# Optimization experiments

Hardware: AMD Instinct MI355X
Metric: run time of the kernel (lower is better)

## Reference

```python
import jax, jax.numpy as jnp
import numpy as np

D = 1024
B = 16384

def setup_inputs() -> dict:
    key = jax.random.key(0)
    ks = jax.random.split(key, 8)
    s = 1.0 / np.sqrt(D)  # torch Linear default init scale (uniform), use scaled normal
    return {
        "f1": jax.random.normal(ks[0], (B, D), jnp.float32),
        "f2": jax.random.normal(ks[1], (B, D), jnp.float32),
        "Wq": jax.random.normal(ks[2], (D, D), jnp.float32) * s,
        "bq": jax.random.normal(ks[3], (D,), jnp.float32) * s,
        "Wk": jax.random.normal(ks[4], (D, D), jnp.float32) * s,
        "bk": jax.random.normal(ks[5], (D,), jnp.float32) * s,
        "Wv": jax.random.normal(ks[6], (D, D), jnp.float32) * s,
        "bv": jax.random.normal(ks[7], (D,), jnp.float32) * s,
    }

def reference(f1, f2, Wq, bq, Wk, bk, Wv, bv):
    d = f1.shape[-1]
    feats = jnp.stack([f1, f2], axis=1)          # [B, 2, D]
    # nn.Linear: y = x @ W.T + b
    Q = jnp.einsum("bsd,ed->bse", feats, Wq) + bq  # [B, 2, D]
    K = jnp.einsum("bsd,ed->bse", feats, Wk) + bk
    V = jnp.einsum("bsd,ed->bse", feats, Wv) + bv
    scores = jnp.einsum("bse,bte->bst", Q, K) / jnp.sqrt(jnp.asarray(d, feats.dtype))  # [B, 2, 2]
    attn = jax.nn.softmax(scores, axis=-1)
    attended = jnp.einsum("bst,btd->bsd", attn, V)  # [B, 2, D]
    return attended.sum(axis=1)                     # [B, D]
```

## Files before the change

kernel.cpp:

```cpp
#include <hip/hip_runtime.h>
#include <hip/hip_bf16.h>
#include <stdint.h>

typedef unsigned short u16;
typedef __bf16 bf16x8 __attribute__((ext_vector_type(8)));
typedef float f32x4 __attribute__((ext_vector_type(4)));

#define D_DIM 1024
#define B_ROWS 16384
#define M_ROWS 32768
#define BM 128
#define BN 128
#define BK 64

__device__ __forceinline__ u16 f2bs(float f) {
    union { float f; unsigned u; } v; v.f = f;
    unsigned r = v.u + 0x7FFFu + ((v.u >> 16) & 1u);
    return (u16)(r >> 16);
}
__device__ __forceinline__ float bs2f(unsigned bits16) {
    union { unsigned u; float f; } v; v.u = bits16 << 16;
    return v.f;
}
__device__ __forceinline__ float bidx(uint2 v, int e) {
    unsigned w = (e < 2) ? v.x : v.y;
    unsigned sh = (unsigned)(e & 1) * 16u;
    return bs2f((w >> sh) & 0xFFFFu);
}
__device__ __forceinline__ uint2 pack4(float4 f) {
    uint2 r;
    r.x = (unsigned)f2bs(f.x) | ((unsigned)f2bs(f.y) << 16);
    r.y = (unsigned)f2bs(f.z) | ((unsigned)f2bs(f.w) << 16);
    return r;
}

#define GLD16(gsrc, ldst)                                                      \
    __builtin_amdgcn_global_load_lds(                                          \
        (const __attribute__((address_space(1))) void*)(gsrc),                 \
        (__attribute__((address_space(3))) void*)(ldst), 16, 0, 0)

#define MFMA16(a, b, c) __builtin_amdgcn_mfma_f32_16x16x32_bf16((a), (b), (c), 0, 0, 0)

__global__ __launch_bounds__(256) void cvt_feats(const float* __restrict__ f1,
                                                 const float* __restrict__ f2,
                                                 u16* __restrict__ X) {
    size_t i4   = (size_t)blockIdx.x * 256 + threadIdx.x;
    size_t base = i4 * 4;
    size_t brow = base >> 10;
    size_t col  = base & 1023;
    float4 a = *(const float4*)(f1 + base);
    float4 b = *(const float4*)(f2 + base);
    *(uint2*)(X + (2 * brow) * D_DIM + col)     = pack4(a);
    *(uint2*)(X + (2 * brow + 1) * D_DIM + col) = pack4(b);
}

__global__ __launch_bounds__(256) void cvt_wv(const float* __restrict__ Wv,
                                              u16* __restrict__ Wvb) {
    size_t base = ((size_t)blockIdx.x * 256 + threadIdx.x) * 4;
    *(uint2*)(Wvb + base) = pack4(*(const float4*)(Wv + base));
}

__global__ __launch_bounds__(256) void transpose_bf16(const float* __restrict__ in,
                                                      u16* __restrict__ out) {
    __shared__ float lds[32][33];
    const int tx = threadIdx.x & 31;
    const int ty = threadIdx.x >> 5;
    const int r0 = (blockIdx.x >> 5) * 32;
    const int c0 = (blockIdx.x & 31) * 32;
#pragma unroll
    for (int i = 0; i < 4; ++i) {
        int r = ty + i * 8;
        lds[r][tx] = in[(size_t)(r0 + r) * D_DIM + c0 + tx];
    }
    __syncthreads();
#pragma unroll
    for (int i = 0; i < 4; ++i) {
        int r = ty + i * 8;
        out[(size_t)(c0 + r) * D_DIM + r0 + tx] = f2bs(lds[tx][r]);
    }
}

__global__ __launch_bounds__(256) void uvc_k(const float* __restrict__ Wq,
                                             const float* __restrict__ Wk,
                                             const float* __restrict__ bq,
                                             const float* __restrict__ bk,
                                             float* __restrict__ u,
                                             float* __restrict__ v,
                                             float* __restrict__ cbuf) {
    const int dl = threadIdx.x & 31;
    const int fg = threadIdx.x >> 5;
    const int d  = blockIdx.x * 32 + dl;
    float au = 0.f, av = 0.f;
    const int f0 = fg * 128;
    for (int f = f0; f < f0 + 128; ++f) {
        au = fmaf(Wq[(size_t)f * D_DIM + d], bk[f], au);
        av = fmaf(Wk[(size_t)f * D_DIM + d], bq[f], av);
    }
    __shared__ float su[8][32], sv[8][32];
    su[fg][dl] = au; sv[fg][dl] = av;
    __syncthreads();
    if (fg == 0) {
        float a = 0.f, b2 = 0.f;
#pragma unroll
        for (int g = 0; g < 8; ++g) { a += su[g][dl]; b2 += sv[g][dl]; }
        u[d] = a; v[d] = b2;
    }
    if (blockIdx.x == 0) {
        __shared__ float red[256];
        float p = 0.f;
        for (int f = threadIdx.x; f < D_DIM; f += 256) p = fmaf(bq[f], bk[f], p);
        red[threadIdx.x] = p;
        __syncthreads();
        for (int s = 128; s; s >>= 1) {
            if (threadIdx.x < s) red[threadIdx.x] += red[threadIdx.x + s];
            __syncthreads();
        }
        if (threadIdx.x == 0) cbuf[0] = red[0];
    }
}

__global__ __launch_bounds__(256, 3) void gemm_small(const u16* __restrict__ A,
                                                     const u16* __restrict__ W,
                                                     u16* __restrict__ C, int ncols) {
    constexpr int K = D_DIM;
    __shared__ u16 As[BM * BK];
    __shared__ u16 Bs[BN * BK];

    const int cpx  = gridDim.x >> 3;
    const int orig = (blockIdx.x & 7) * cpx + (blockIdx.x >> 3);
    const int nTn = ncols / BN;
    const int m0 = (orig / nTn) * BM, n0 = (orig % nTn) * BN;

    const int tid  = threadIdx.x;
    const int lane = tid & 63;
    const int wave = tid >> 6;
    const int wr = wave >> 1, wc = wave & 1;
    const int lr = lane & 15;
    const int kg = lane >> 4;

    f32x4 acc[4][4] = {};

    const int sr  = tid >> 3;
    const int scs = ((tid & 7) ^ ((tid >> 3) & 7)) * 8;
    const u16* aRow = A + (size_t)(m0 + sr) * K + scs;
    const u16* bRow = W + (size_t)(n0 + sr) * K + scs;
    u16* aDst = As + tid * 8;
    u16* bDst = Bs + tid * 8;

    for (int kt = 0; kt < K; kt += BK) {
#pragma unroll
        for (int i = 0; i < 4; ++i) {
            GLD16(aRow + (size_t)i * 32 * K + kt, aDst + i * 2048);
            GLD16(bRow + (size_t)i * 32 * K + kt, bDst + i * 2048);
        }
        __syncthreads();
#pragma unroll
        for (int kk = 0; kk < 2; ++kk) {
            bf16x8 af[4], bfr[4];
            const int kx = kk * 4 + kg;
#pragma unroll
            for (int mf = 0; mf < 4; ++mf) {
                const int R = wr * 64 + mf * 16 + lr;
                af[mf] = *(const bf16x8*)(As + R * 64 + ((kx ^ (R & 7)) * 8));
            }
#pragma unroll
            for (int nf = 0; nf < 4; ++nf) {
                const int S = wc * 64 + nf * 16 + lr;
                bfr[nf] = *(const bf16x8*)(Bs + S * 64 + ((kx ^ (S & 7)) * 8));
            }
#pragma unroll
            for (int mf = 0; mf < 4; ++mf)
#pragma unroll
                for (int nf = 0; nf < 4; ++nf)
                    acc[mf][nf] = MFMA16(af[mf], bfr[nf], acc[mf][nf]);
        }
        __syncthreads();
    }

    const int cr = (lane >> 4) * 4;
    const int cc = lane & 15;
#pragma unroll
    for (int mf = 0; mf < 4; ++mf)
#pragma unroll
        for (int nf = 0; nf < 4; ++nf) {
            int col = n0 + wc * 64 + nf * 16 + cc;
#pragma unroll
            for (int j = 0; j < 4; ++j) {
                int row = m0 + wr * 64 + mf * 16 + cr + j;
                C[(size_t)row * ncols + col] = f2bs(acc[mf][nf][j]);
            }
        }
}

template<bool FUSED>
__global__ __launch_bounds__(512, 2) void gemm8p(const u16* __restrict__ A,
                                                 const u16* __restrict__ W,
                                                 const float* __restrict__ bias,
                                                 u16* __restrict__ C,
                                                 const float2* __restrict__ wts,
                                                 float* __restrict__ out,
                                                 int ncols) {
    constexpr int K  = D_DIM;
    constexpr int NT = K / 64;
    __shared__ u16 L[65536];

    const int cpx  = gridDim.x >> 3;
    const int orig = (blockIdx.x & 7) * cpx + (blockIdx.x >> 3);
    const int nTn  = ncols >> 8;
    const int m0 = (orig / nTn) << 8, n0 = (orig % nTn) << 8;

    const int tid  = threadIdx.x;
    const int lane = tid & 63;
    const int wid  = tid >> 6;
    const int wm = wid >> 2, wn = wid & 3;
    const int lr = lane & 15;
    const int kg = lane >> 4;
    const int r7 = lr & 7;
    const int cx0 = ((0 + kg) ^ r7) * 8;
    const int cx1 = ((4 + kg) ^ r7) * 8;
    const int sS  = (wn & 1) * 64;

    const int rb  = tid >> 3;
    const int scs = ((tid & 7) ^ (rb & 7)) * 8;
    const u16* aB = A + (size_t)(m0 + rb) * K + scs;
    const u16* bB = W + (size_t)(n0 + rb) * K + scs;
    u16* aD = L + tid * 8;
    u16* bD = L + 32768 + tid * 8;

#define ST_HALF(tile, h)                                                       \
    {                                                                          \
        const int d_ = (tile) & 1;                                             \
        const size_t ko_ = (size_t)(tile) * 64;                                \
        if ((h) < 2) {                                                         \
            const u16* s_ = aB + (size_t)(h) * 128 * K + ko_;                  \
            u16* t_ = aD + (d_ * 2 + (h)) * 8192;                              \
            GLD16(s_, t_);                                                     \
            GLD16(s_ + (size_t)64 * K, t_ + 4096);                            \
        } else {                                                               \
            const u16* s_ = bB + (size_t)((h) - 2) * 128 * K + ko_;            \
            u16* t_ = bD + (d_ * 2 + ((h) - 2)) * 8192;                        \
            GLD16(s_, t_);                                                     \
            GLD16(s_ + (size_t)64 * K, t_ + 4096);                            \
        }                                                                      \
    }

    f32x4 acc[8][4] = {};
    bf16x8 af[8][2], bf[4][2];

#pragma unroll
    for (int h = 0; h < 4; ++h) ST_HALF(0, h);
#pragma unroll
    for (int h = 0; h < 4; ++h) ST_HALF(1, h);
    asm volatile("s_waitcnt vmcnt(8)" ::: "memory");
    __builtin_amdgcn_s_barrier();

#pragma unroll 2
    for (int t = 0; t < NT; ++t) {
        const int d = t & 1;
        const u16* Ab = L + (d * 2 + wm) * 8192;
        const u16* Bb = L + 32768 + (d * 2 + (wn >> 1)) * 8192;
        const bool more = (t + 2 < NT);

#pragma unroll
        for (int m = 0; m < 4; ++m) {
            const int R = m * 16 + lr;
            af[m][0] = *(const bf16x8*)(Ab + R * 64 + cx0);
            af[m][1] = *(const bf16x8*)(Ab + R * 64 + cx1);
        }
#pragma unroll
        for (int n = 0; n < 2; ++n) {
            const int S = sS + n * 16 + lr;
            bf[n][0] = *(const bf16x8*)(Bb + S * 64 + cx0);
            bf[n][1] = *(const bf16x8*)(Bb + S * 64 + cx1);
        }
        __builtin_amdgcn_s_barrier();
        __builtin_amdgcn_s_setprio(1);
#pragma unroll
        for (int m = 0; m < 4; ++m)
#pragma unroll
            for (int n = 0; n < 2; ++n) {
                acc[m][n] = MFMA16(af[m][0], bf[n][0], acc[m][n]);
                acc[m][n] = MFMA16(af[m][1], bf[n][1], acc[m][n]);
            }
        __builtin_amdgcn_s_setprio(0);
        __builtin_amdgcn_s_barrier();

#pragma unroll
        for (int n = 2; n < 4; ++n) {
            const int S = sS + n * 16 + lr;
            bf[n][0] = *(const bf16x8*)(Bb + S * 64 + cx0);
            bf[n][1] = *(const bf16x8*)(Bb + S * 64 + cx1);
        }
        __builtin_amdgcn_s_barrier();
        __builtin_amdgcn_s_setprio(1);
#pragma unroll
        for (int m = 0; m < 4; ++m)
#pragma unroll
            for (int n = 2; n < 4; ++n) {
                acc[m][n] = MFMA16(af[m][0], bf[n][0], acc[m][n]);
                acc[m][n] = MFMA16(af[m][1], bf[n][1], acc[m][n]);
            }
        __builtin_amdgcn_s_setprio(0);
        __builtin_amdgcn_s_barrier();

#pragma unroll
        for (int m = 4; m < 8; ++m) {
            const int R = m * 16 + lr;
            af[m][0] = *(const bf16x8*)(Ab + R * 64 + cx0);
            af[m][1] = *(const bf16x8*)(Ab + R * 64 + cx1);
        }
        if (more) { ST_HALF(t + 2, 2); ST_HALF(t + 2, 3); }
        __builtin_amdgcn_s_barrier();
        __builtin_amdgcn_s_setprio(1);
#pragma unroll
        for (int m = 4; m < 8; ++m)
#pragma unroll
            for (int n = 0; n < 2; ++n) {
                acc[m][n] = MFMA16(af[m][0], bf[n][0], acc[m][n]);
                acc[m][n] = MFMA16(af[m][1], bf[n][1], acc[m][n]);
            }
        __builtin_amdgcn_s_setprio(0);
        __builtin_amdgcn_s_barrier();

        if (more) { ST_HALF(t + 2, 0); ST_HALF(t + 2, 1); }
        __builtin_amdgcn_s_barrier();
        __builtin_amdgcn_s_setprio(1);
#pragma unroll
        for (int m = 4; m < 8; ++m)
#pragma unroll
            for (int n = 2; n < 4; ++n) {
                acc[m][n] = MFMA16(af[m][0], bf[n][0], acc[m][n]);
                acc[m][n] = MFMA16(af[m][1], bf[n][1], acc[m][n]);
            }
        __builtin_amdgcn_s_setprio(0);
        if (more) asm volatile("s_waitcnt vmcnt(8)" ::: "memory");
        else      asm volatile("s_waitcnt vmcnt(0)" ::: "memory");
        __builtin_amdgcn_s_barrier();
    }
#undef ST_HALF

    const int cr = (lane >> 4) * 4;
    const int cc = lane & 15;
    if constexpr (!FUSED) {
#pragma unroll
        for (int mf = 0; mf < 8; ++mf)
#pragma unroll
            for (int nf = 0; nf < 4; ++nf) {
                int col = n0 + wn * 64 + nf * 16 + cc;
                float bsv = bias ? bias[col] : 0.f;
#pragma unroll
                for (int j = 0; j < 4; ++j) {
                    int row = m0 + wm * 128 + mf * 16 + cr + j;
                    C[(size_t)row * ncols + col] = f2bs(acc[mf][nf][j] + bsv);
                }
            }
    } else {
#pragma unroll
        for (int mf = 0; mf < 8; ++mf) {
            const int rowbase = m0 + wm * 128 + mf * 16 + cr;
            const int p0 = rowbase >> 1;
            const float2 w0 = wts[p0];
            const float2 w1 = wts[p0 + 1];
#pragma unroll
            for (int nf = 0; nf < 4; ++nf) {
                int col = n0 + wn * 64 + nf * 16 + cc;
                float bsv = bias[col];
                float o0 = w0.x * (acc[mf][nf][0] + bsv) + w0.y * (acc[mf][nf][1] + bsv);
                float o1 = w1.x * (acc[mf][nf][2] + bsv) + w1.y * (acc[mf][nf][3] + bsv);
                out[(size_t)p0 * D_DIM + col]       = o0;
                out[(size_t)(p0 + 1) * D_DIM + col] = o1;
            }
        }
    }
}

__global__ __launch_bounds__(256) void scores2(const u16* __restrict__ X,
                                               const u16* __restrict__ G,
                                               const float* __restrict__ u,
                                               const float* __restrict__ v,
                                               const float* __restrict__ cbuf,
                                               float2* __restrict__ wts) {
    const int wave = threadIdx.x >> 6;
    const int lane = threadIdx.x & 63;
    const size_t b = (size_t)blockIdx.x * 4 + wave;
    const u16* x0p = X + (2 * b) * D_DIM;
    const u16* x1p = x0p + D_DIM;
    const u16* g0p = G + (2 * b) * D_DIM;
    const u16* g1p = g0p + D_DIM;

    float d00 = 0.f, d01 = 0.f, d10 = 0.f, d11 = 0.f;
    float au0 = 0.f, au1 = 0.f, bv0 = 0.f, bv1 = 0.f;
#pragma unroll
    for (int s = 0; s < 4; ++s) {
        int c = s * 256 + lane * 4;
        uint2 x0 = *(const uint2*)(x0p + c);
        uint2 x1 = *(const uint2*)(x1p + c);
        uint2 g0 = *(const uint2*)(g0p + c);
        uint2 g1 = *(const uint2*)(g1p + c);
        float4 uu = *(const float4*)(u + c);
        float4 vv = *(const float4*)(v + c);
        float uA[4] = {uu.x, uu.y, uu.z, uu.w};
        float vA[4] = {vv.x, vv.y, vv.z, vv.w};
#pragma unroll
        for (int e = 0; e < 4; ++e) {
            float a0 = bidx(x0, e), a1 = bidx(x1, e);
            float c0 = bidx(g0, e), c1 = bidx(g1, e);
            d00 = fmaf(a0, c0, d00); d01 = fmaf(a0, c1, d01);
            d10 = fmaf(a1, c0, d10); d11 = fmaf(a1, c1, d11);
            au0 = fmaf(uA[e], a0, au0); au1 = fmaf(uA[e], a1, au1);
            bv0 = fmaf(vA[e], a0, bv0); bv1 = fmaf(vA[e], a1, bv1);
        }
    }
#pragma unroll
    for (int off = 32; off; off >>= 1) {
        d00 += __shfl_xor(d00, off); d01 += __shfl_xor(d01, off);
        d10 += __shfl_xor(d10, off); d11 += __shfl_xor(d11, off);
        au0 += __shfl_xor(au0, off); au1 += __shfl_xor(au1, off);
        bv0 += __shfl_xor(bv0, off); bv1 += __shfl_xor(bv1, off);
    }
    if (lane == 0) {
        const float cc0 = cbuf[0];
        const float sc = 1.0f / 32.0f;
        float s00 = (d00 + au0 + bv0 + cc0) * sc;
        float s01 = (d01 + au0 + bv1 + cc0) * sc;
        float s10 = (d10 + au1 + bv0 + cc0) * sc;
        float s11 = (d11 + au1 + bv1 + cc0) * sc;
        float mA = fmaxf(s00, s01);
        float e00 = expf(s00 - mA), e01 = expf(s01 - mA);
        float rA = 1.0f / (e00 + e01);
        float mB = fmaxf(s10, s11);
        float e10 = expf(s10 - mB), e11 = expf(s11 - mB);
        float rB = 1.0f / (e10 + e11);
        float2 w;
        w.x = e00 * rA + e10 * rB;
        w.y = e01 * rA + e11 * rB;
        wts[b] = w;
    }
}

extern "C" void kernel_launch(void* const* d_in, const int* in_sizes, int n_in,
                              void* d_out, int out_size, void* d_ws, size_t ws_size,
                              hipStream_t stream) {
    const float* f1 = (const float*)d_in[0];
    const float* f2 = (const float*)d_in[1];
    const float* Wq = (const float*)d_in[2];
    const float* bq = (const float*)d_in[3];
    const float* Wk = (const float*)d_in[4];
    const float* bk = (const float*)d_in[5];
    const float* Wv = (const float*)d_in[6];
    const float* bv = (const float*)d_in[7];
    float* out = (float*)d_out;

    char*   w    = (char*)d_ws;
    u16*    X    = (u16*)w;
    u16*    G    = X + (size_t)M_ROWS * D_DIM;
    u16*    Wvb  = G + (size_t)M_ROWS * D_DIM;
    u16*    WqT  = Wvb + (size_t)D_DIM * D_DIM;
    u16*    WkT  = WqT + (size_t)D_DIM * D_DIM;
    u16*    Mb   = WkT + (size_t)D_DIM * D_DIM;
    float*  u    = (float*)(Mb + (size_t)D_DIM * D_DIM);
    float*  v    = u + D_DIM;
    float*  cbuf = v + D_DIM;
    float2* wts  = (float2*)(cbuf + 64);

    cvt_feats<<<(B_ROWS * D_DIM / 4) / 256, 256, 0, stream>>>(f1, f2, X);
    cvt_wv<<<(D_DIM * D_DIM / 4) / 256, 256, 0, stream>>>(Wv, Wvb);
    transpose_bf16<<<1024, 256, 0, stream>>>(Wq, WqT);
    transpose_bf16<<<1024, 256, 0, stream>>>(Wk, WkT);
    uvc_k<<<D_DIM / 32, 256, 0, stream>>>(Wq, Wk, bq, bk, u, v, cbuf);

    gemm_small<<<(D_DIM / BM) * (D_DIM / BN), 256, 0, stream>>>(WqT, WkT, Mb, D_DIM);
    gemm8p<false><<<(M_ROWS / 256) * (D_DIM / 256), 512, 0, stream>>>(
        X, Mb, nullptr, G, nullptr, nullptr, D_DIM);
    scores2<<<B_ROWS / 4, 256, 0, stream>>>(X, G, u, v, cbuf, wts);
    gemm8p<true><<<(M_ROWS / 256) * (D_DIM / 256), 512, 0, stream>>>(
        X, Wvb, bv, nullptr, wts, out, D_DIM);
}
```

Measured before the change: 227.3 us.

## Mix feature rows by attention weights before V projection to halve V GEMM

Because the output is linear in V, the scores kernel now forms Z = w0*x0 + w1*x1 per batch row in bf16. The V projection then runs on B rows instead of 2B rows, with the bias added as 2*bv. This roughly halves the second large GEMM's FLOPs and removes the weighted fused epilogue. It costs an extra B×D bf16 write and read of Z, plus an additional bf16 rounding of the mixed features.

```diff
diff --git a/kernel.cpp b/kernel.cpp
--- a/kernel.cpp
+++ b/kernel.cpp
@@ -22,10 +22,9 @@
     union { unsigned u; float f; } v; v.u = bits16 << 16;
     return v.f;
 }
-__device__ __forceinline__ float bidx(uint2 v, int e) {
-    unsigned w = (e < 2) ? v.x : v.y;
-    unsigned sh = (unsigned)(e & 1) * 16u;
-    return bs2f((w >> sh) & 0xFFFFu);
+__device__ __forceinline__ float b8x(uint4 q, int e) {
+    unsigned w[4] = {q.x, q.y, q.z, q.w};
+    return bs2f((w[e >> 1] >> ((unsigned)(e & 1) * 16u)) & 0xFFFFu);
 }
 __device__ __forceinline__ uint2 pack4(float4 f) {
     uint2 r;
@@ -192,12 +191,11 @@
         }
 }
 
-template<bool FUSED>
+template<bool F32OUT>
 __global__ __launch_bounds__(512, 2) void gemm8p(const u16* __restrict__ A,
                                                  const u16* __restrict__ W,
                                                  const float* __restrict__ bias,
                                                  u16* __restrict__ C,
-                                                 const float2* __restrict__ wts,
                                                  float* __restrict__ out,
                                                  int ncols) {
     constexpr int K  = D_DIM;
@@ -341,45 +339,40 @@
 
     const int cr = (lane >> 4) * 4;
     const int cc = lane & 15;
-    if constexpr (!FUSED) {
+    if constexpr (!F32OUT) {
 #pragma unroll
         for (int mf = 0; mf < 8; ++mf)
 #pragma unroll
             for (int nf = 0; nf < 4; ++nf) {
                 int col = n0 + wn * 64 + nf * 16 + cc;
-                float bsv = bias ? bias[col] : 0.f;
 #pragma unroll
                 for (int j = 0; j < 4; ++j) {
                     int row = m0 + wm * 128 + mf * 16 + cr + j;
-                    C[(size_t)row * ncols + col] = f2bs(acc[mf][nf][j] + bsv);
+                    C[(size_t)row * ncols + col] = f2bs(acc[mf][nf][j]);
                 }
             }
     } else {
 #pragma unroll
-        for (int mf = 0; mf < 8; ++mf) {
-            const int rowbase = m0 + wm * 128 + mf * 16 + cr;
-            const int p0 = rowbase >> 1;
-            const float2 w0 = wts[p0];
-            const float2 w1 = wts[p0 + 1];
+        for (int mf = 0; mf < 8; ++mf)
 #pragma unroll
             for (int nf = 0; nf < 4; ++nf) {
                 int col = n0 + wn * 64 + nf * 16 + cc;
-                float bsv = bias[col];
-                float o0 = w0.x * (acc[mf][nf][0] + bsv) + w0.y * (acc[mf][nf][1] + bsv);
-                float o1 = w1.x * (acc[mf][nf][2] + bsv) + w1.y * (acc[mf][nf][3] + bsv);
-                out[(size_t)p0 * D_DIM + col]       = o0;
-                out[(size_t)(p0 + 1) * D_DIM + col] = o1;
-            }
-        }
-    }
-}
-
-__global__ __launch_bounds__(256) void scores2(const u16* __restrict__ X,
-                                               const u16* __restrict__ G,
-                                               const float* __restrict__ u,
-                                               const float* __restrict__ v,
-                                               const float* __restrict__ cbuf,
-                                               float2* __restrict__ wts) {
+                float bsv = 2.0f * bias[col];
+#pragma unroll
+                for (int j = 0; j < 4; ++j) {
+                    int row = m0 + wm * 128 + mf * 16 + cr + j;
+                    out[(size_t)row * ncols + col] = acc[mf][nf][j] + bsv;
+                }
+            }
+    }
+}
+
+__global__ __launch_bounds__(256) void scores_z(const u16* __restrict__ X,
+                                                const u16* __restrict__ G,
+                                                const float* __restrict__ u,
+                                                const float* __restrict__ v,
+                                                const float* __restrict__ cbuf,
+                                                u16* __restrict__ Z) {
     const int wave = threadIdx.x >> 6;
     const int lane = threadIdx.x & 63;
     const size_t b = (size_t)blockIdx.x * 4 + wave;
@@ -390,21 +383,24 @@
 
     float d00 = 0.f, d01 = 0.f, d10 = 0.f, d11 = 0.f;
     float au0 = 0.f, au1 = 0.f, bv0 = 0.f, bv1 = 0.f;
-#pragma unroll
-    for (int s = 0; s < 4; ++s) {
-        int c = s * 256 + lane * 4;
-        uint2 x0 = *(const uint2*)(x0p + c);
-        uint2 x1 = *(const uint2*)(x1p + c);
-        uint2 g0 = *(const uint2*)(g0p + c);
-        uint2 g1 = *(const uint2*)(g1p + c);
-        float4 uu = *(const float4*)(u + c);
-        float4 vv = *(const float4*)(v + c);
-        float uA[4] = {uu.x, uu.y, uu.z, uu.w};
-        float vA[4] = {vv.x, vv.y, vv.z, vv.w};
-#pragma unroll
-        for (int e = 0; e < 4; ++e) {
-            float a0 = bidx(x0, e), a1 = bidx(x1, e);
-            float c0 = bidx(g0, e), c1 = bidx(g1, e);
+    uint4 x0c[2], x1c[2];
+#pragma unroll
+    for (int s = 0; s < 2; ++s) {
+        const int c = s * 512 + lane * 8;
+        x0c[s] = *(const uint4*)(x0p + c);
+        x1c[s] = *(const uint4*)(x1p + c);
+        uint4 g0 = *(const uint4*)(g0p + c);
+        uint4 g1 = *(const uint4*)(g1p + c);
+        float4 uuA = *(const float4*)(u + c);
+        float4 uuB = *(const float4*)(u + c + 4);
+        float4 vvA = *(const float4*)(v + c);
+        float4 vvB = *(const float4*)(v + c + 4);
+        float uA[8] = {uuA.x, uuA.y, uuA.z, uuA.w, uuB.x, uuB.y, uuB.z, uuB.w};
+        float vA[8] = {vvA.x, vvA.y, vvA.z, vvA.w, vvB.x, vvB.y, vvB.z, vvB.w};
+#pragma unroll
+        for (int e = 0; e < 8; ++e) {
+            float a0 = b8x(x0c[s], e), a1 = b8x(x1c[s], e);
+            float c0 = b8x(g0, e),     c1 = b8x(g1, e);
             d00 = fmaf(a0, c0, d00); d01 = fmaf(a0, c1, d01);
             d10 = fmaf(a1, c0, d10); d11 = fmaf(a1, c1, d11);
             au0 = fmaf(uA[e], a0, au0); au1 = fmaf(uA[e], a1, au1);
@@ -418,23 +414,36 @@
         au0 += __shfl_xor(au0, off); au1 += __shfl_xor(au1, off);
         bv0 += __shfl_xor(bv0, off); bv1 += __shfl_xor(bv1, off);
     }
-    if (lane == 0) {
-        const float cc0 = cbuf[0];
-        const float sc = 1.0f / 32.0f;
-        float s00 = (d00 + au0 + bv0 + cc0) * sc;
-        float s01 = (d01 + au0 + bv1 + cc0) * sc;
-        float s10 = (d10 + au1 + bv0 + cc0) * sc;
-        float s11 = (d11 + au1 + bv1 + cc0) * sc;
-        float mA = fmaxf(s00, s01);
-        float e00 = expf(s00 - mA), e01 = expf(s01 - mA);
-        float rA = 1.0f / (e00 + e01);
-        float mB = fmaxf(s10, s11);
-        float e10 = expf(s10 - mB), e11 = expf(s11 - mB);
-        float rB = 1.0f / (e10 + e11);
-        float2 w;
-        w.x = e00 * rA + e10 * rB;
-        w.y = e01 * rA + e11 * rB;
-        wts[b] = w;
+    const float cc0 = cbuf[0];
+    const float sc = 1.0f / 32.0f;
+    float s00 = (d00 + au0 + bv0 + cc0) * sc;
+    float s01 = (d01 + au0 + bv1 + cc0) * sc;
+    float s10 = (d10 + au1 + bv0 + cc0) * sc;
+    float s11 = (d11 + au1 + bv1 + cc0) * sc;
+    float mA = fmaxf(s00, s01);
+    float e00 = expf(s00 - mA), e01 = expf(s01 - mA);
+    float rA = 1.0f / (e00 + e01);
+    float mB = fmaxf(s10, s11);
+    float e10 = expf(s10 - mB), e11 = expf(s11 - mB);
+    float rB = 1.0f / (e10 + e11);
+    const float w0 = e00 * rA + e10 * rB;
+    const float w1 = e01 * rA + e11 * rB;
+
+#pragma unroll
+    for (int s = 0; s < 2; ++s) {
+        const int c = s * 512 + lane * 8;
+        float4 lo, hi;
+        lo.x = w0 * b8x(x0c[s], 0) + w1 * b8x(x1c[s], 0);
+        lo.y = w0 * b8x(x0c[s], 1) + w1 * b8x(x1c[s], 1);
+        lo.z = w0 * b8x(x0c[s], 2) + w1 * b8x(x1c[s], 2);
+        lo.w = w0 * b8x(x0c[s], 3) + w1 * b8x(x1c[s], 3);
+        hi.x = w0 * b8x(x0c[s], 4) + w1 * b8x(x1c[s], 4);
+        hi.y = w0 * b8x(x0c[s], 5) + w1 * b8x(x1c[s], 5);
+        hi.z = w0 * b8x(x0c[s], 6) + w1 * b8x(x1c[s], 6);
+        hi.w = w0 * b8x(x0c[s], 7) + w1 * b8x(x1c[s], 7);
+        uint2 pl = pack4(lo), ph = pack4(hi);
+        uint4 o; o.x = pl.x; o.y = pl.y; o.z = ph.x; o.w = ph.y;
+        *(uint4*)(Z + b * D_DIM + c) = o;
     }
 }
 
@@ -454,14 +463,14 @@
     char*   w    = (char*)d_ws;
     u16*    X    = (u16*)w;
     u16*    G    = X + (size_t)M_ROWS * D_DIM;
-    u16*    Wvb  = G + (size_t)M_ROWS * D_DIM;
+    u16*    Z    = G + (size_t)M_ROWS * D_DIM;
+    u16*    Wvb  = Z + (size_t)B_ROWS * D_DIM;
     u16*    WqT  = Wvb + (size_t)D_DIM * D_DIM;
     u16*    WkT  = WqT + (size_t)D_DIM * D_DIM;
     u16*    Mb   = WkT + (size_t)D_DIM * D_DIM;
     float*  u    = (float*)(Mb + (size_t)D_DIM * D_DIM);
     float*  v    = u + D_DIM;
     float*  cbuf = v + D_DIM;
-    float2* wts  = (float2*)(cbuf + 64);
 
     cvt_feats<<<(B_ROWS * D_DIM / 4) / 256, 256, 0, stream>>>(f1, f2, X);
     cvt_wv<<<(D_DIM * D_DIM / 4) / 256, 256, 0, stream>>>(Wv, Wvb);
@@ -471,8 +480,8 @@
 
     gemm_small<<<(D_DIM / BM) * (D_DIM / BN), 256, 0, stream>>>(WqT, WkT, Mb, D_DIM);
     gemm8p<false><<<(M_ROWS / 256) * (D_DIM / 256), 512, 0, stream>>>(
-        X, Mb, nullptr, G, nullptr, nullptr, D_DIM);
-    scores2<<<B_ROWS / 4, 256, 0, stream>>>(X, G, u, v, cbuf, wts);
-    gemm8p<true><<<(M_ROWS / 256) * (D_DIM / 256), 512, 0, stream>>>(
-        X, Wvb, bv, nullptr, wts, out, D_DIM);
-}
+        X, Mb, nullptr, G, nullptr, D_DIM);
+    scores_z<<<B_ROWS / 4, 256, 0, stream>>>(X, G, u, v, cbuf, Z);
+    gemm8p<true><<<(B_ROWS / 256) * (D_DIM / 256), 512, 0, stream>>>(
+        Z, Wvb, bv, nullptr, out, D_DIM);
+}
```

After: 204.7 us. 1.11x faster.
